# Kernel optimization log

Measured on AMD Instinct MI355X. Metric: run time of the kernel, lower is better.

## Reference

```python
import jax, jax.numpy as jnp
import numpy as np

N, IN_DIM, OUT_DIM = 8192, 512, 256


def setup_inputs() -> dict:
    key = jax.random.key(0)
    k1, k2, k3 = jax.random.split(key, 3)
    X = jax.random.normal(k1, (N, IN_DIM), dtype=jnp.float32)
    # torch nn.Linear(in_dim, out_dim, bias=False): y = x @ W^T; store as [in_dim, out_dim]
    W = jax.random.normal(k2, (IN_DIM, OUT_DIM), dtype=jnp.float32) / np.sqrt(IN_DIM)
    # a: Linear(2*out_dim, 1, bias=False) -> vector of length 2*out_dim
    a = jax.random.normal(k3, (2 * OUT_DIM,), dtype=jnp.float32) / np.sqrt(2 * OUT_DIM)
    return {"X": X, "W": W, "a": a}


def reference(X, W, a):
    H = X @ W  # [N, D]
    D = H.shape[1]
    # a([Hi ; Hj]) = Hi @ a[:D] + Hj @ a[D:] -> avoid materializing [N,N,2D]
    e = (H @ a[:D])[:, None] + (H @ a[D:])[None, :]  # [N, N]
    e = jnp.where(e > 0, e, 0.2 * e)  # leaky_relu(0.2)
    A = jax.nn.softmax(e, axis=-1)  # row softmax [N, N]
    out = A @ H  # [N, D]
    return out, A
```

## Files before the change

### kernel.cpp

```cpp
#include <hip/hip_runtime.h>
#include <math.h>

#define NN 8192
#define KDIM 512
#define DD 256
#define CS 32
#define NC 256

typedef float4 f4;
typedef __attribute__((ext_vector_type(4))) float f4v;

__global__ __launch_bounds__(256) void k_gemm(const float* __restrict__ X,
                                              const float* __restrict__ W,
                                              float* __restrict__ H) {
  __shared__ float Xs[32][64];
  __shared__ float Ws[32][64];
  const int tid = threadIdx.x;
  const int tx = tid & 15;
  const int ty = tid >> 4;
  const int r0 = blockIdx.x * 64;
  const int c0 = blockIdx.y * 64;
  float acc[4][4] = {};
  for (int k0 = 0; k0 < KDIM; k0 += 32) {
#pragma unroll
    for (int q = 0; q < 2; ++q) {
      int fi = tid + q * 256;
      int r = fi >> 3;
      int kq = fi & 7;
      f4 v = *reinterpret_cast<const f4*>(&X[(size_t)(r0 + r) * KDIM + k0 + kq * 4]);
      Xs[kq * 4 + 0][r] = v.x; Xs[kq * 4 + 1][r] = v.y;
      Xs[kq * 4 + 2][r] = v.z; Xs[kq * 4 + 3][r] = v.w;
    }
#pragma unroll
    for (int q = 0; q < 2; ++q) {
      int fi = tid + q * 256;
      int k = fi >> 4;
      int cq = fi & 15;
      f4 v = *reinterpret_cast<const f4*>(&W[(size_t)(k0 + k) * DD + c0 + cq * 4]);
      *reinterpret_cast<f4*>(&Ws[k][cq * 4]) = v;
    }
    __syncthreads();
#pragma unroll
    for (int k = 0; k < 32; ++k) {
      f4 xv = *reinterpret_cast<const f4*>(&Xs[k][ty * 4]);
      f4 wv = *reinterpret_cast<const f4*>(&Ws[k][tx * 4]);
      float xs[4] = {xv.x, xv.y, xv.z, xv.w};
      float ws[4] = {wv.x, wv.y, wv.z, wv.w};
#pragma unroll
      for (int i = 0; i < 4; ++i)
#pragma unroll
        for (int j = 0; j < 4; ++j) acc[i][j] += xs[i] * ws[j];
    }
    __syncthreads();
  }
#pragma unroll
  for (int i = 0; i < 4; ++i) {
    f4 v = {acc[i][0], acc[i][1], acc[i][2], acc[i][3]};
    *reinterpret_cast<f4*>(&H[(size_t)(r0 + ty * 4 + i) * DD + c0 + tx * 4]) = v;
  }
}

__global__ __launch_bounds__(256) void k_rowdots(const float* __restrict__ H,
                                                 const float* __restrict__ a,
                                                 float* __restrict__ s,
                                                 float* __restrict__ t,
                                                 float* __restrict__ E1,
                                                 float* __restrict__ E2) {
  int wid = threadIdx.x >> 6;
  int lane = threadIdx.x & 63;
  int i = blockIdx.x * 4 + wid;
  f4 h  = *reinterpret_cast<const f4*>(&H[(size_t)i * DD + lane * 4]);
  f4 a1 = *reinterpret_cast<const f4*>(&a[lane * 4]);
  f4 a2 = *reinterpret_cast<const f4*>(&a[DD + lane * 4]);
  float p1 = h.x * a1.x + h.y * a1.y + h.z * a1.z + h.w * a1.w;
  float p2 = h.x * a2.x + h.y * a2.y + h.z * a2.z + h.w * a2.w;
  for (int off = 32; off > 0; off >>= 1) {
    p1 += __shfl_down(p1, off);
    p2 += __shfl_down(p2, off);
  }
  if (lane == 0) {
    s[i] = p1;
    t[i] = p2;
    E1[i] = expf(p2);
    E2[i] = expf(0.2f * p2);
  }
}

__global__ __launch_bounds__(1024) void k_tmax_coef(const float* __restrict__ s,
                                                    const float* __restrict__ t,
                                                    float* __restrict__ c1,
                                                    float* __restrict__ c2) {
  __shared__ float red[16];
  int tid = threadIdx.x;
  float m = -1e30f;
  for (int k = tid; k < NN; k += 1024) m = fmaxf(m, t[k]);
  for (int off = 32; off > 0; off >>= 1) m = fmaxf(m, __shfl_down(m, off));
  if ((tid & 63) == 0) red[tid >> 6] = m;
  __syncthreads();
  if (tid < 16) {
    float v = red[tid];
    for (int off = 8; off > 0; off >>= 1) v = fmaxf(v, __shfl_down(v, off));
    if (tid == 0) red[0] = v;
  }
  __syncthreads();
  float tmax = red[0];
  for (int k = tid; k < NN; k += 1024) {
    float si = s[k];
    float e = si + tmax;
    float mm = e > 0.f ? e : 0.2f * e;
    c1[k] = expf(si - mm);
    c2[k] = expf(0.2f * si - mm);
  }
}

__global__ __launch_bounds__(1024) void k_sort(const float* __restrict__ t,
                                               float* __restrict__ tsort,
                                               int* __restrict__ perm) {
  __shared__ float v[NN];
  __shared__ int ix[NN];
  int tid = threadIdx.x;
  for (int k = tid; k < NN; k += 1024) { v[k] = t[k]; ix[k] = k; }
  for (int size = 2; size <= NN; size <<= 1) {
    for (int stride = size >> 1; stride > 0; stride >>= 1) {
      __syncthreads();
      for (int p = tid; p < NN / 2; p += 1024) {
        int i = ((p & ~(stride - 1)) << 1) | (p & (stride - 1));
        int j = i | stride;
        bool asc = (i & size) == 0;
        float vi = v[i], vj = v[j];
        bool sw = asc ? (vi > vj) : (vi < vj);
        if (sw) {
          v[i] = vj; v[j] = vi;
          int tmp = ix[i]; ix[i] = ix[j]; ix[j] = tmp;
        }
      }
    }
  }
  __syncthreads();
  for (int k = tid; k < NN; k += 1024) { tsort[k] = v[k]; perm[k] = ix[k]; }
}

__global__ __launch_bounds__(256) void k_chunk(const float* __restrict__ H,
                                               const float* __restrict__ E1,
                                               const float* __restrict__ E2,
                                               const int* __restrict__ perm,
                                               float* __restrict__ Ctot1,
                                               float* __restrict__ Ctot2,
                                               float* __restrict__ cs1,
                                               float* __restrict__ cs2) {
  int c = blockIdx.x;
  int d = threadIdx.x;
  float s1 = 0.f, s2 = 0.f, a1 = 0.f, a2 = 0.f;
  for (int kk = 0; kk < CS; ++kk) {
    int p = perm[c * CS + kk];
    float e1 = E1[p], e2 = E2[p];
    float h = H[(size_t)p * DD + d];
    s1 += e1 * h; s2 += e2 * h;
    a1 += e1;     a2 += e2;
  }
  Ctot1[c * DD + d] = s1;
  Ctot2[c * DD + d] = s2;
  if (d == 0) { cs1[c] = a1; cs2[c] = a2; }
}

__global__ __launch_bounds__(256) void k_scan(const float* __restrict__ Ctot1,
                                              const float* __restrict__ Ctot2,
                                              float* __restrict__ Coff1,
                                              float* __restrict__ Coff2,
                                              const float* __restrict__ cs1,
                                              const float* __restrict__ cs2,
                                              float* __restrict__ cso1,
                                              float* __restrict__ cso2) {
  int d = threadIdx.x;
  float r1 = 0.f, r2 = 0.f;
  for (int c = 0; c < NC; ++c) {
    Coff1[c * DD + d] = r1; r1 += Ctot1[c * DD + d];
    Coff2[c * DD + d] = r2; r2 += Ctot2[c * DD + d];
  }
  __shared__ float sv1[NC], sv2[NC];
  float x1 = cs1[d], x2 = cs2[d];
  sv1[d] = x1; sv2[d] = x2;
  __syncthreads();
  for (int off = 1; off < NC; off <<= 1) {
    float y1 = (d >= off) ? sv1[d - off] : 0.f;
    float y2 = (d >= off) ? sv2[d - off] : 0.f;
    __syncthreads();
    sv1[d] += y1; sv2[d] += y2;
    __syncthreads();
  }
  cso1[d] = (d == 0) ? 0.f : sv1[d - 1];
  cso2[d] = (d == 0) ? 0.f : sv2[d - 1];
}

__global__ __launch_bounds__(256) void k_prefix(const float* __restrict__ H,
                                                const float* __restrict__ E1,
                                                const float* __restrict__ E2,
                                                const int* __restrict__ perm,
                                                const float* __restrict__ Coff1,
                                                const float* __restrict__ Coff2,
                                                const float* __restrict__ cso1,
                                                const float* __restrict__ cso2,
                                                float* __restrict__ PRE1,
                                                float* __restrict__ PRE2,
                                                float* __restrict__ p1s,
                                                float* __restrict__ p2s) {
  int c = blockIdx.x;
  int d = threadIdx.x;
  float r1 = Coff1[c * DD + d], r2 = Coff2[c * DD + d];
  float sr1 = 0.f, sr2 = 0.f;
  if (d == 0) { sr1 = cso1[c]; sr2 = cso2[c]; }
  for (int kk = 0; kk < CS; ++kk) {
    int k = c * CS + kk;
    int p = perm[k];
    PRE1[(size_t)k * DD + d] = r1;
    PRE2[(size_t)k * DD + d] = r2;
    float e1 = E1[p], e2 = E2[p];
    float h = H[(size_t)p * DD + d];
    r1 += e1 * h; r2 += e2 * h;
    if (d == 0) { p1s[k] = sr1; p2s[k] = sr2; sr1 += e1; sr2 += e2; }
  }
  if (c == NC - 1) {
    PRE1[(size_t)NN * DD + d] = r1;
    PRE2[(size_t)NN * DD + d] = r2;
    if (d == 0) { p1s[NN] = sr1; p2s[NN] = sr2; }
  }
}

__global__ __launch_bounds__(256) void k_finalize(const float* __restrict__ s,
                                                  const float* __restrict__ c1,
                                                  const float* __restrict__ c2,
                                                  const float* __restrict__ tsort,
                                                  const float* __restrict__ p1s,
                                                  const float* __restrict__ p2s,
                                                  const float* __restrict__ PRE1,
                                                  const float* __restrict__ PRE2,
                                                  float* __restrict__ out,
                                                  float* __restrict__ f1,
                                                  float* __restrict__ f2) {
  int wid = threadIdx.x >> 6, lane = threadIdx.x & 63;
  int i = blockIdx.x * 4 + wid;
  float key = -s[i];
  int lo = 0, hi = NN;
  while (lo < hi) {
    int mid = (lo + hi) >> 1;
    if (tsort[mid] <= key) lo = mid + 1; else hi = mid;
  }
  int k = lo;
  float cc1 = c1[i], cc2 = c2[i];
  float Z = cc1 * (p1s[NN] - p1s[k]) + cc2 * p2s[k];
  float rZ = 1.0f / Z;
  if (lane == 0) { f1[i] = rZ * cc1; f2[i] = rZ * cc2; }
  int d = lane * 4;
  f4 P1 = *reinterpret_cast<const f4*>(&PRE1[(size_t)k * DD + d]);
  f4 P2 = *reinterpret_cast<const f4*>(&PRE2[(size_t)k * DD + d]);
  f4 T1 = *reinterpret_cast<const f4*>(&PRE1[(size_t)NN * DD + d]);
  f4 o;
  o.x = rZ * (cc1 * (T1.x - P1.x) + cc2 * P2.x);
  o.y = rZ * (cc1 * (T1.y - P1.y) + cc2 * P2.y);
  o.z = rZ * (cc1 * (T1.z - P1.z) + cc2 * P2.z);
  o.w = rZ * (cc1 * (T1.w - P1.w) + cc2 * P2.w);
  *reinterpret_cast<f4*>(&out[(size_t)i * DD + d]) = o;
}

__global__ __launch_bounds__(256) void k_astream(const float* __restrict__ s,
                                                 const float* __restrict__ t,
                                                 const float* __restrict__ E1,
                                                 const float* __restrict__ E2,
                                                 const float* __restrict__ f1,
                                                 const float* __restrict__ f2,
                                                 float* __restrict__ A) {
  int j0 = blockIdx.x * 1024 + threadIdx.x * 4;
  int i0 = blockIdx.y * 32;
  f4 t4  = *reinterpret_cast<const f4*>(&t[j0]);
  f4 e14 = *reinterpret_cast<const f4*>(&E1[j0]);
  f4 e24 = *reinterpret_cast<const f4*>(&E2[j0]);
#pragma unroll 4
  for (int rr = 0; rr < 32; ++rr) {
    int i = i0 + rr;
    float ss = s[i], ff1 = f1[i], ff2 = f2[i];
    f4v o;
    float e;
    e = ss + t4.x; o.x = (e > 0.f) ? ff1 * e14.x : ff2 * e24.x;
    e = ss + t4.y; o.y = (e > 0.f) ? ff1 * e14.y : ff2 * e24.y;
    e = ss + t4.z; o.z = (e > 0.f) ? ff1 * e14.z : ff2 * e24.z;
    e = ss + t4.w; o.w = (e > 0.f) ? ff1 * e14.w : ff2 * e24.w;
    __builtin_nontemporal_store(o, reinterpret_cast<f4v*>(&A[(size_t)i * NN + j0]));
  }
}

extern "C" void kernel_launch(void* const* d_in, const int* in_sizes, int n_in,
                              void* d_out, int out_size, void* d_ws, size_t ws_size,
                              hipStream_t stream) {
  const float* X = (const float*)d_in[0];
  const float* W = (const float*)d_in[1];
  const float* a = (const float*)d_in[2];
  float* out = (float*)d_out;
  float* A = out + (size_t)NN * DD;

  float* ws = (float*)d_ws;
  float* s  = ws + 0 * NN;
  float* t  = ws + 1 * NN;
  float* E1 = ws + 2 * NN;
  float* E2 = ws + 3 * NN;
  float* c1 = ws + 4 * NN;
  float* c2 = ws + 5 * NN;
  float* f1 = ws + 6 * NN;
  float* f2 = ws + 7 * NN;

  float* H     = out;
  float* PRE1  = A;
  float* PRE2  = A + 4194304;
  float* Ctot1 = A + 8388608;
  float* Ctot2 = Ctot1 + NC * DD;
  float* Coff1 = Ctot2 + NC * DD;
  float* Coff2 = Coff1 + NC * DD;
  float* cs1   = Coff2 + NC * DD;
  float* cs2   = cs1 + NC;
  float* cso1  = cs2 + NC;
  float* cso2  = cso1 + NC;
  float* p1s   = cso2 + NC;
  float* p2s   = p1s + (NN + 256);
  float* tsort = p2s + (NN + 256);
  int*   perm  = (int*)(tsort + NN);

  k_gemm<<<dim3(NN / 64, DD / 64), 256, 0, stream>>>(X, W, H);
  k_rowdots<<<NN / 4, 256, 0, stream>>>(H, a, s, t, E1, E2);
  k_tmax_coef<<<1, 1024, 0, stream>>>(s, t, c1, c2);
  k_sort<<<1, 1024, 0, stream>>>(t, tsort, perm);
  k_chunk<<<NC, 256, 0, stream>>>(H, E1, E2, perm, Ctot1, Ctot2, cs1, cs2);
  k_scan<<<1, 256, 0, stream>>>(Ctot1, Ctot2, Coff1, Coff2, cs1, cs2, cso1, cso2);
  k_prefix<<<NC, 256, 0, stream>>>(H, E1, E2, perm, Coff1, Coff2, cso1, cso2,
                                   PRE1, PRE2, p1s, p2s);
  k_finalize<<<NN / 4, 256, 0, stream>>>(s, c1, c2, tsort, p1s, p2s, PRE1, PRE2,
                                         out, f1, f2);
  k_astream<<<dim3(NN / 1024, NN / 32), 256, 0, stream>>>(s, t, E1, E2, f1, f2, A);
}
```

Before: 224.6 us.

## Replace single-block bitonic sort with parallel rank sort and fold scan into prefix

The single-workgroup bitonic sort of 8192 keys is replaced by a two-kernel rank sort: 256 blocks each count, for every key, how many of their 32 keys precede it, and a second kernel sums these partial counts and scatters each key to its rank. The one-block chunk-offset scan kernel is removed; each prefix block instead sums the preceding chunk totals and reduces the chunk scalar sums itself. This removes two serial single-block stages from the dependency chain, in exchange for O(N^2) comparisons, an 8 MB partial-count buffer, and redundant per-block summation in the prefix kernel.

```diff
diff --git a/kernel.cpp b/kernel.cpp
--- a/kernel.cpp
+++ b/kernel.cpp
@@ -6,6 +6,8 @@
 #define DD 256
 #define CS 32
 #define NC 256
+#define RKB 32
+#define NBK (NN / RKB)
 
 typedef float4 f4;
 typedef __attribute__((ext_vector_type(4))) float f4v;
@@ -113,31 +115,38 @@
   }
 }
 
-__global__ __launch_bounds__(1024) void k_sort(const float* __restrict__ t,
-                                               float* __restrict__ tsort,
-                                               int* __restrict__ perm) {
-  __shared__ float v[NN];
-  __shared__ int ix[NN];
+__global__ __launch_bounds__(256) void k_rank_partial(const float* __restrict__ t,
+                                                      int* __restrict__ Pcnt) {
+  int b = blockIdx.x;
   int tid = threadIdx.x;
-  for (int k = tid; k < NN; k += 1024) { v[k] = t[k]; ix[k] = k; }
-  for (int size = 2; size <= NN; size <<= 1) {
-    for (int stride = size >> 1; stride > 0; stride >>= 1) {
-      __syncthreads();
-      for (int p = tid; p < NN / 2; p += 1024) {
-        int i = ((p & ~(stride - 1)) << 1) | (p & (stride - 1));
-        int j = i | stride;
-        bool asc = (i & size) == 0;
-        float vi = v[i], vj = v[j];
-        bool sw = asc ? (vi > vj) : (vi < vj);
-        if (sw) {
-          v[i] = vj; v[j] = vi;
-          int tmp = ix[i]; ix[i] = ix[j]; ix[j] = tmp;
-        }
-      }
+  __shared__ float tk[RKB];
+  if (tid < RKB) tk[tid] = t[b * RKB + tid];
+  __syncthreads();
+#pragma unroll
+  for (int q = 0; q < NN / 256; ++q) {
+    int j = q * 256 + tid;
+    float tj = t[j];
+    int cnt = 0;
+#pragma unroll
+    for (int kk = 0; kk < RKB; ++kk) {
+      int kg = b * RKB + kk;
+      float tv = tk[kk];
+      cnt += (tv < tj) || (tv == tj && kg < j);
     }
-  }
-  __syncthreads();
-  for (int k = tid; k < NN; k += 1024) { tsort[k] = v[k]; perm[k] = ix[k]; }
+    Pcnt[(size_t)b * NN + j] = cnt;
+  }
+}
+
+__global__ __launch_bounds__(256) void k_rank_scatter(const float* __restrict__ t,
+                                                      const int* __restrict__ Pcnt,
+                                                      float* __restrict__ tsort,
+                                                      int* __restrict__ perm) {
+  int j = blockIdx.x * 256 + threadIdx.x;
+  int r = 0;
+#pragma unroll 8
+  for (int b = 0; b < NBK; ++b) r += Pcnt[(size_t)b * NN + j];
+  tsort[r] = t[j];
+  perm[r] = j;
 }
 
 __global__ __launch_bounds__(256) void k_chunk(const float* __restrict__ H,
@@ -163,52 +172,34 @@
   if (d == 0) { cs1[c] = a1; cs2[c] = a2; }
 }
 
-__global__ __launch_bounds__(256) void k_scan(const float* __restrict__ Ctot1,
-                                              const float* __restrict__ Ctot2,
-                                              float* __restrict__ Coff1,
-                                              float* __restrict__ Coff2,
-                                              const float* __restrict__ cs1,
-                                              const float* __restrict__ cs2,
-                                              float* __restrict__ cso1,
-                                              float* __restrict__ cso2) {
-  int d = threadIdx.x;
-  float r1 = 0.f, r2 = 0.f;
-  for (int c = 0; c < NC; ++c) {
-    Coff1[c * DD + d] = r1; r1 += Ctot1[c * DD + d];
-    Coff2[c * DD + d] = r2; r2 += Ctot2[c * DD + d];
-  }
-  __shared__ float sv1[NC], sv2[NC];
-  float x1 = cs1[d], x2 = cs2[d];
-  sv1[d] = x1; sv2[d] = x2;
-  __syncthreads();
-  for (int off = 1; off < NC; off <<= 1) {
-    float y1 = (d >= off) ? sv1[d - off] : 0.f;
-    float y2 = (d >= off) ? sv2[d - off] : 0.f;
-    __syncthreads();
-    sv1[d] += y1; sv2[d] += y2;
-    __syncthreads();
-  }
-  cso1[d] = (d == 0) ? 0.f : sv1[d - 1];
-  cso2[d] = (d == 0) ? 0.f : sv2[d - 1];
-}
-
 __global__ __launch_bounds__(256) void k_prefix(const float* __restrict__ H,
                                                 const float* __restrict__ E1,
                                                 const float* __restrict__ E2,
                                                 const int* __restrict__ perm,
-                                                const float* __restrict__ Coff1,
-                                                const float* __restrict__ Coff2,
-                                                const float* __restrict__ cso1,
-                                                const float* __restrict__ cso2,
+                                                const float* __restrict__ Ctot1,
+                                                const float* __restrict__ Ctot2,
+                                                const float* __restrict__ cs1,
+                                                const float* __restrict__ cs2,
                                                 float* __restrict__ PRE1,
                                                 float* __restrict__ PRE2,
                                                 float* __restrict__ p1s,
                                                 float* __restrict__ p2s) {
   int c = blockIdx.x;
   int d = threadIdx.x;
-  float r1 = Coff1[c * DD + d], r2 = Coff2[c * DD + d];
-  float sr1 = 0.f, sr2 = 0.f;
-  if (d == 0) { sr1 = cso1[c]; sr2 = cso2[c]; }
+  float r1 = 0.f, r2 = 0.f;
+  for (int cc = 0; cc < c; ++cc) {
+    r1 += Ctot1[cc * DD + d];
+    r2 += Ctot2[cc * DD + d];
+  }
+  __shared__ float sa[NC], sb[NC];
+  sa[d] = (d < c) ? cs1[d] : 0.f;
+  sb[d] = (d < c) ? cs2[d] : 0.f;
+  __syncthreads();
+  for (int off = 128; off > 0; off >>= 1) {
+    if (d < off) { sa[d] += sa[d + off]; sb[d] += sb[d + off]; }
+    __syncthreads();
+  }
+  float sr1 = sa[0], sr2 = sb[0];
   for (int kk = 0; kk < CS; ++kk) {
     int k = c * CS + kk;
     int p = perm[k];
@@ -312,24 +303,21 @@
   float* PRE2  = A + 4194304;
   float* Ctot1 = A + 8388608;
   float* Ctot2 = Ctot1 + NC * DD;
-  float* Coff1 = Ctot2 + NC * DD;
-  float* Coff2 = Coff1 + NC * DD;
-  float* cs1   = Coff2 + NC * DD;
+  float* cs1   = Ctot2 + NC * DD;
   float* cs2   = cs1 + NC;
-  float* cso1  = cs2 + NC;
-  float* cso2  = cso1 + NC;
-  float* p1s   = cso2 + NC;
+  float* p1s   = cs2 + NC;
   float* p2s   = p1s + (NN + 256);
   float* tsort = p2s + (NN + 256);
   int*   perm  = (int*)(tsort + NN);
+  int*   Pcnt  = (int*)(perm + NN);
 
   k_gemm<<<dim3(NN / 64, DD / 64), 256, 0, stream>>>(X, W, H);
   k_rowdots<<<NN / 4, 256, 0, stream>>>(H, a, s, t, E1, E2);
   k_tmax_coef<<<1, 1024, 0, stream>>>(s, t, c1, c2);
-  k_sort<<<1, 1024, 0, stream>>>(t, tsort, perm);
+  k_rank_partial<<<NBK, 256, 0, stream>>>(t, Pcnt);
+  k_rank_scatter<<<NN / 256, 256, 0, stream>>>(t, Pcnt, tsort, perm);
   k_chunk<<<NC, 256, 0, stream>>>(H, E1, E2, perm, Ctot1, Ctot2, cs1, cs2);
-  k_scan<<<1, 256, 0, stream>>>(Ctot1, Ctot2, Coff1, Coff2, cs1, cs2, cso1, cso2);
-  k_prefix<<<NC, 256, 0, stream>>>(H, E1, E2, perm, Coff1, Coff2, cso1, cso2,
+  k_prefix<<<NC, 256, 0, stream>>>(H, E1, E2, perm, Ctot1, Ctot2, cs1, cs2,
                                    PRE1, PRE2, p1s, p2s);
   k_finalize<<<NN / 4, 256, 0, stream>>>(s, c1, c2, tsort, p1s, p2s, PRE1, PRE2,
                                          out, f1, f2);
```

Measured after the change: 229.8 us. 2.3% more time.
